# Performance work log

Hardware: AMD Instinct MI355X
Metric: run time of the kernel (lower is better)

## Reference

```python
import jax, jax.numpy as jnp
import numpy as np

N_USER = 100000
N_ITEM = 50000
N = N_USER + N_ITEM
D = 64
E = 4000000
B = 4096
NUM_LAYERS = 2
INT_W = 0.1
POP_W = 0.1
DIS_PEN = 0.01


def setup_inputs() -> dict:
    key = jax.random.key(0)
    ks = jax.random.split(key, 8)
    stdv = 1.0 / np.sqrt(D).astype(np.float32)
    emb_int = jax.random.uniform(ks[0], (N, D), minval=-stdv, maxval=stdv, dtype=jnp.float32)
    emb_pop = jax.random.uniform(ks[1], (N, D), minval=-stdv, maxval=stdv, dtype=jnp.float32)
    user = jax.random.randint(ks[2], (B, 1), 0, N_USER)
    item_p = jax.random.randint(ks[3], (B, 1), 0, N_ITEM)
    item_n = jax.random.randint(ks[4], (B, 1), 0, N_ITEM)
    mask = jax.random.randint(ks[5], (B, 1), 0, 2).astype(bool)
    src = jax.random.randint(ks[6], (E,), 0, N)
    dst = jax.random.randint(ks[7], (E,), 0, N)
    return {"emb_int": emb_int, "emb_pop": emb_pop, "user": user, "item_p": item_p,
            "item_n": item_n, "mask": mask, "src": src, "dst": dst}


def _propagate(emb, src, dst, norm):
    # LightGCN: mean over layer-0..L embeddings, each layer = norm * A @ (norm * h)
    feats = emb
    h = emb
    for _ in range(NUM_LAYERS):
        h = h * norm
        h = jax.ops.segment_sum(h[src], dst, num_segments=N)  # copy_u / sum
        h = h * norm
        feats = feats + h  # dropout p=0 -> identity
    return feats / (NUM_LAYERS + 1)


def reference(emb_int, emb_pop, user, item_p, item_n, mask, src, dst):
    deg = jax.ops.segment_sum(jnp.ones((E,), jnp.float32), dst, num_segments=N)
    norm = jnp.maximum(deg, 1.0) ** -0.5  # [N]
    norm = norm[:, None]  # [N,1]

    f_int = _propagate(emb_int, src, dst, norm)
    f_pop = _propagate(emb_pop, src, dst, norm)

    ip = item_p + N_USER
    inn = item_n + N_USER

    u_int, u_pop = f_int[user], f_pop[user]          # [B,1,D]
    p_int = jnp.sum(u_int * f_int[ip], axis=2)        # [B,1]
    n_int = jnp.sum(u_int * f_int[inn], axis=2)
    p_pop = jnp.sum(u_pop * f_pop[ip], axis=2)
    n_pop = jnp.sum(u_pop * f_pop[inn], axis=2)

    ls = jax.nn.log_sigmoid
    mf = mask.astype(jnp.float32)
    loss_int = -jnp.mean(mf * ls(p_int - n_int))
    loss_pop = -jnp.mean(mf * ls(n_pop - p_pop)) - jnp.mean((1.0 - mf) * ls(p_pop - n_pop))
    loss_total = -jnp.mean(ls((p_int + p_pop) - (n_int + n_pop)))

    # MSE over unique gathered rows == indicator-weighted mean over the table
    item_ind = jnp.zeros((N,), jnp.float32).at[ip.ravel()].set(1.0).at[inn.ravel()].set(1.0)
    user_ind = jnp.zeros((N,), jnp.float32).at[user.ravel()].set(1.0)
    diff2 = (f_int - f_pop) ** 2
    def mse(ind):
        return jnp.sum(ind[:, None] * diff2) / (jnp.sum(ind) * D)
    discrepancy = mse(item_ind) + mse(user_ind)

    return jnp.stack([loss_total, INT_W * loss_int, POP_W * loss_pop, -DIS_PEN * discrepancy])
```

## Files before the change

### kernel.cpp

```cpp
#include <hip/hip_runtime.h>
#include <hip/hip_bf16.h>

typedef unsigned int u32;
typedef float f32x2 __attribute__((ext_vector_type(2)));

#define KNODES 512
#define KSHIFT 9
#define NBMAX 1024
#define CHUNK 4096
#define CAP 16384

__device__ __forceinline__ float log_sigmoid(float x) {
    return fminf(x, 0.f) - log1pf(expf(-fabsf(x)));
}

template <bool HI>
__device__ __forceinline__ f32x2 up8(u32 v) {
    return __builtin_amdgcn_cvt_pk_f32_fp8(v, HI);
}
template <bool HI>
__device__ __forceinline__ u32 pk8(u32 old, float a, float b) {
    return __builtin_amdgcn_cvt_pk_fp8_f32(a, b, old, HI);
}

__global__ void __launch_bounds__(512)
k_scatter(const int* __restrict__ src, const int* __restrict__ dst,
          u32* __restrict__ tails, u32* __restrict__ packed, int E, int nb,
          const int* __restrict__ user, const int* __restrict__ itp,
          const int* __restrict__ itn,
          float* __restrict__ item_ind, float* __restrict__ user_ind,
          int B, int NUSER, const int* __restrict__ maskw, int* __restrict__ flag) {
    __shared__ u32 h[NBMAX];
    const int t = threadIdx.x;
    const int base = blockIdx.x * CHUNK;
    const int PT = CHUNK / 512;
    u32 dv[PT], sv[PT];
#pragma unroll
    for (int i = 0; i < PT; ++i) {
        int e = base + t + i * 512;
        if (e < E) { dv[i] = (u32)dst[e]; sv[i] = (u32)src[e]; }
        else dv[i] = 0xFFFFFFFFu;
    }
    for (int i = t; i < nb; i += 512) h[i] = 0;
    __syncthreads();
#pragma unroll
    for (int i = 0; i < PT; ++i)
        if (dv[i] != 0xFFFFFFFFu) atomicAdd(&h[dv[i] >> KSHIFT], 1u);
    __syncthreads();
    for (int i = t; i < nb; i += 512) {
        u32 c = h[i];
        if (c) h[i] = ((u32)i * CAP) + atomicAdd(&tails[i], c);
    }
    __syncthreads();
#pragma unroll
    for (int i = 0; i < PT; ++i) {
        if (dv[i] != 0xFFFFFFFFu) {
            u32 b = dv[i] >> KSHIFT;
            u32 pos = atomicAdd(&h[b], 1u);
            if (pos < (b + 1u) * CAP)
                packed[pos] = ((dv[i] & (KNODES - 1)) << 18) | sv[i];
        }
    }
    int gid = blockIdx.x * blockDim.x + t;
    int stride = gridDim.x * blockDim.x;
    for (int b = gid; b < B; b += stride) {
        item_ind[itp[b] + NUSER] = 1.f;
        item_ind[itn[b] + NUSER] = 1.f;
        user_ind[user[b]] = 1.f;
    }
    if (blockIdx.x == 0) {
        __shared__ int allok;
        if (t == 0) allok = 1;
        __syncthreads();
        bool ok = true;
        for (int i = t; i < 1024; i += 512) {
            int v = maskw[i];
            if (v != 0 && v != 1) ok = false;
        }
        if (!ok) allok = 0;
        __syncthreads();
        if (t == 0) flag[0] = allok;
    }
}

__global__ void __launch_bounds__(1024)
k_bbuild(const u32* __restrict__ packed, const u32* __restrict__ tails,
         uint2* __restrict__ rowrange, float* __restrict__ norm,
         float* __restrict__ norm2, float* __restrict__ snorm,
         int* __restrict__ csr, int N) {
    __shared__ u32 deg[KNODES], fill[KNODES], sc[KNODES];
    const int t = threadIdx.x;
    const int bkt = blockIdx.x;
    const int nodeBase = bkt << KSHIFT;
    const u32 e0 = (u32)bkt * CAP;
    const u32 e1 = e0 + tails[bkt];
    if (t < KNODES) deg[t] = 0;
    __syncthreads();
    for (u32 e = e0 + t; e < e1; e += 1024)
        atomicAdd(&deg[packed[e] >> 18], 1u);
    __syncthreads();
    u32 dv = (t < KNODES) ? deg[t] : 0u;
    if (t < KNODES) sc[t] = dv;
    __syncthreads();
    for (int off = 1; off < KNODES; off <<= 1) {
        u32 x = 0;
        if (t < KNODES && t >= off) x = sc[t - off];
        __syncthreads();
        if (t < KNODES) sc[t] += x;
        __syncthreads();
    }
    if (t < KNODES) {
        u32 ebase = sc[t] - dv;
        fill[t] = ebase;
        int n = nodeBase + t;
        if (n < N) {
            float dd = fmaxf((float)dv, 1.f);
            float nr = rsqrtf(dd);
            rowrange[n] = make_uint2(e0 + ebase, e0 + ebase + dv);
            norm[n] = nr;
            norm2[n] = nr * nr;
            snorm[n] = sqrtf(dd) * (1.f / 64.f);
        }
    }
    __syncthreads();
    for (u32 e = e0 + t; e < e1; e += 1024) {
        u32 p = packed[e];
        u32 ln = p >> 18;
        u32 pos = atomicAdd(&fill[ln], 1u);
        csr[e0 + pos] = (int)(p & 0x3FFFFu);
    }
}

__global__ void k_pack(const float* __restrict__ eI, const float* __restrict__ eP,
                       const float* __restrict__ norm, u32* __restrict__ T0, int N) {
    int idx = blockIdx.x * blockDim.x + threadIdx.x;
    int total = N * 32;
    int stride = gridDim.x * blockDim.x;
    for (; idx < total; idx += stride) {
        int n = idx >> 5, k = idx & 31;
        const float* e = (k >= 16) ? eP : eI;
        int d0 = (4 * k) & 63;
        float4 v = *(const float4*)&e[(size_t)n * 64 + d0];
        float s = 64.f * norm[n];
        u32 w = 0;
        w = pk8<false>(w, v.x * s, v.y * s);
        w = pk8<true>(w, v.z * s, v.w * s);
        T0[idx] = w;
    }
}

#define ACC8(u) { f32x2 p0 = up8<false>(u.x), p1 = up8<true>(u.x); \
                  f32x2 p2 = up8<false>(u.y), p3 = up8<true>(u.y); \
                  a0 += p0.x; a1 += p0.y; a2 += p1.x; a3 += p1.y;  \
                  a4 += p2.x; a5 += p2.y; a6 += p3.x; a7 += p3.y; }

__global__ void k_pull(const u32* __restrict__ Tin, u32* __restrict__ Tout,
                       const int* __restrict__ csr, const uint2* __restrict__ rowrange,
                       const float* __restrict__ norm2, int N) {
    int lane = threadIdx.x & 63;
    int grp = lane >> 4;
    int r = lane & 15;
    int wid = (blockIdx.x * blockDim.x + threadIdx.x) >> 6;
    int nw = (gridDim.x * blockDim.x) >> 6;
    for (int n = wid; n < N; n += nw) {
        uint2 rr = rowrange[n];
        u32 s0 = rr.x, s1 = rr.y;
        float a0 = 0.f, a1 = 0.f, a2 = 0.f, a3 = 0.f, a4 = 0.f, a5 = 0.f, a6 = 0.f, a7 = 0.f;
        for (u32 e0 = s0; e0 < s1; e0 += 64) {
            int cnt = (int)min(64u, s1 - e0);
            int sidx = (lane < cnt) ? csr[e0 + lane] : 0;
            int j = 0;
            for (; j + 8 <= cnt; j += 8) {
                int sA = __shfl(sidx, j + grp);
                int sB = __shfl(sidx, j + 4 + grp);
                uint2 uA = *(const uint2*)&Tin[(size_t)sA * 32 + 2 * r];
                uint2 uB = *(const uint2*)&Tin[(size_t)sB * 32 + 2 * r];
                ACC8(uA); ACC8(uB);
            }
            for (; j + 4 <= cnt; j += 4) {
                int sA = __shfl(sidx, j + grp);
                uint2 uA = *(const uint2*)&Tin[(size_t)sA * 32 + 2 * r];
                ACC8(uA);
            }
            int rem = cnt - j;
            if (rem) {
                int jj = j + grp;
                int s = __shfl(sidx, (jj < cnt) ? jj : 0);
                if (grp < rem) {
                    uint2 u = *(const uint2*)&Tin[(size_t)s * 32 + 2 * r];
                    ACC8(u);
                }
            }
        }
        a0 += __shfl_xor(a0, 16); a1 += __shfl_xor(a1, 16);
        a2 += __shfl_xor(a2, 16); a3 += __shfl_xor(a3, 16);
        a4 += __shfl_xor(a4, 16); a5 += __shfl_xor(a5, 16);
        a6 += __shfl_xor(a6, 16); a7 += __shfl_xor(a7, 16);
        a0 += __shfl_xor(a0, 32); a1 += __shfl_xor(a1, 32);
        a2 += __shfl_xor(a2, 32); a3 += __shfl_xor(a3, 32);
        a4 += __shfl_xor(a4, 32); a5 += __shfl_xor(a5, 32);
        a6 += __shfl_xor(a6, 32); a7 += __shfl_xor(a7, 32);
        float nn = norm2[n];
        if (lane < 16) {
            u32 w0 = 0, w1 = 0;
            w0 = pk8<false>(w0, a0 * nn, a1 * nn);
            w0 = pk8<true>(w0, a2 * nn, a3 * nn);
            w1 = pk8<false>(w1, a4 * nn, a5 * nn);
            w1 = pk8<true>(w1, a6 * nn, a7 * nn);
            uint2 w; w.x = w0; w.y = w1;
            *(uint2*)&Tout[(size_t)n * 32 + 2 * r] = w;
        }
    }
}

__device__ __forceinline__ void fval2(const float* __restrict__ eb,
                                      const u32* __restrict__ T1, const u32* __restrict__ T2,
                                      const float* __restrict__ snorm,
                                      int r, int toff, int lh, float& f0, float& f1) {
    float2 ev = *(const float2*)&eb[(size_t)r * 64 + 2 * lh];
    u32 w1 = T1[(size_t)r * 32 + toff + (lh >> 1)];
    u32 w2 = T2[(size_t)r * 32 + toff + (lh >> 1)];
    bool hi = lh & 1;
    f32x2 t1 = hi ? up8<true>(w1) : up8<false>(w1);
    f32x2 t2 = hi ? up8<true>(w2) : up8<false>(w2);
    float sr = snorm[r];
    f0 = (ev.x + sr * (t1.x + t2.x)) * (1.f / 3.f);
    f1 = (ev.y + sr * (t1.y + t2.y)) * (1.f / 3.f);
}

__global__ void k_tail(const float* __restrict__ eI, const float* __restrict__ eP,
                       const u32* __restrict__ T1, const u32* __restrict__ T2,
                       const float* __restrict__ snorm,
                       const int* __restrict__ user, const int* __restrict__ itp, const int* __restrict__ itn,
                       const void* __restrict__ maskp, const int* __restrict__ flag,
                       const float* __restrict__ item_ind, const float* __restrict__ user_ind,
                       float* __restrict__ bpart,
                       int B, int NUSER, int N, int Lb, int totalBlocks) {
    __shared__ float part[4][4];
    int lane = threadIdx.x & 63;
    int wib = threadIdx.x >> 6;
    int half = lane >> 5, lh = lane & 31;
    int toff = half ? 16 : 0;
    const float* eb = half ? eP : eI;
    float* row = &bpart[(size_t)blockIdx.x * 8];
    if ((int)blockIdx.x < Lb) {
        int b = (blockIdx.x * blockDim.x + threadIdx.x) >> 6;
        float r0 = 0.f, r1 = 0.f, r2 = 0.f;
        if (b < B) {
            int u = user[b];
            int ip = itp[b] + NUSER;
            int in_ = itn[b] + NUSER;
            float u0, u1, p0, p1, n0, n1;
            fval2(eb, T1, T2, snorm, u,   toff, lh, u0, u1);
            fval2(eb, T1, T2, snorm, ip,  toff, lh, p0, p1);
            fval2(eb, T1, T2, snorm, in_, toff, lh, n0, n1);
            float dp = u0 * p0 + u1 * p1;
            float dn = u0 * n0 + u1 * n1;
            for (int off = 1; off < 32; off <<= 1) {
                dp += __shfl_xor(dp, off);
                dn += __shfl_xor(dn, off);
            }
            float dpI = __shfl(dp, 0), dpP = __shfl(dp, 32);
            float dnI = __shfl(dn, 0), dnP = __shfl(dn, 32);
            if (lane == 0) {
                float m = (*flag) ? (float)(((const int*)maskp)[b] != 0)
                                  : (float)(((const unsigned char*)maskp)[b] != 0);
                r0 = log_sigmoid(dpI + dpP - dnI - dnP);
                r1 = m * log_sigmoid(dpI - dnI);
                r2 = m * log_sigmoid(dnP - dpP) + (1.f - m) * log_sigmoid(dpP - dnP);
            }
        }
        if (lane == 0) { part[wib][0] = r0; part[wib][1] = r1; part[wib][2] = r2; }
        __syncthreads();
        if (threadIdx.x == 0) {
            float s0 = 0.f, s1 = 0.f, s2 = 0.f;
            for (int w = 0; w < 4; ++w) { s0 += part[w][0]; s1 += part[w][1]; s2 += part[w][2]; }
            row[0] = s0; row[1] = s1; row[2] = s2;
            row[3] = 0.f; row[4] = 0.f; row[5] = 0.f; row[6] = 0.f; row[7] = 0.f;
        }
    } else {
        int bid2 = blockIdx.x - Lb;
        int nDb = totalBlocks - Lb;
        int wch = (bid2 * blockDim.x + threadIdx.x) >> 6;
        int nwv = (nDb * blockDim.x) >> 6;
        int nchunks = (N + 63) >> 6;
        float sI = 0.f, sU = 0.f, cI = 0.f, cU = 0.f;
        for (int c = wch; c < nchunks; c += nwv) {
            int base = c << 6;
            int nl = base + lane;
            float ii = (nl < N) ? item_ind[nl] : 0.f;
            float ui = (nl < N) ? user_ind[nl] : 0.f;
            unsigned long long m = __ballot(ii + ui != 0.f);
            while (m) {
                int b = __ffsll((unsigned long long)m) - 1;
                m &= m - 1;
                int n = base + b;
                float iib = __shfl(ii, b);
                float uib = __shfl(ui, b);
                float f0, f1;
                fval2(eb, T1, T2, snorm, n, toff, lh, f0, f1);
                float o0 = __shfl_xor(f0, 32), o1 = __shfl_xor(f1, 32);
                float d0 = f0 - o0, d1 = f1 - o1;
                float dd = d0 * d0 + d1 * d1;
                sI += iib * dd; sU += uib * dd;
                if (lane == 0) { cI += iib; cU += uib; }
            }
        }
        for (int off = 1; off < 64; off <<= 1) { sI += __shfl_xor(sI, off); sU += __shfl_xor(sU, off); }
        if (lane == 0) { part[wib][0] = 0.5f * sI; part[wib][1] = cI; part[wib][2] = 0.5f * sU; part[wib][3] = cU; }
        __syncthreads();
        if (threadIdx.x == 0) {
            float a = 0.f, b = 0.f, c = 0.f, d = 0.f;
            for (int w = 0; w < 4; ++w) { a += part[w][0]; b += part[w][1]; c += part[w][2]; d += part[w][3]; }
            row[0] = 0.f; row[1] = 0.f; row[2] = 0.f;
            row[3] = a; row[4] = b; row[5] = c; row[6] = d; row[7] = 0.f;
        }
    }
}

__global__ void __launch_bounds__(512)
k_final(const float* __restrict__ bpart, float* __restrict__ out, int B, int nblocks) {
    __shared__ float chans[8];
    int lane = threadIdx.x & 63;
    int w = threadIdx.x >> 6;
    if (w < 7) {
        float s = 0.f;
        for (int k = lane; k < nblocks; k += 64)
            s += bpart[(size_t)k * 8 + w];
        for (int off = 1; off < 64; off <<= 1) s += __shfl_xor(s, off);
        if (lane == 0) chans[w] = s;
    }
    __syncthreads();
    if (threadIdx.x == 0) {
        float invB = 1.f / (float)B;
        out[0] = -chans[0] * invB;
        out[1] = -0.1f * chans[1] * invB;
        out[2] = -0.1f * chans[2] * invB;
        float disc = chans[3] / (fmaxf(chans[4], 1.f) * 64.f) + chans[5] / (fmaxf(chans[6], 1.f) * 64.f);
        out[3] = -0.01f * disc;
    }
}

extern "C" void kernel_launch(void* const* d_in, const int* in_sizes, int n_in,
                              void* d_out, int out_size, void* d_ws, size_t ws_size,
                              hipStream_t stream) {
    const float* emb_int = (const float*)d_in[0];
    const float* emb_pop = (const float*)d_in[1];
    const int* user   = (const int*)d_in[2];
    const int* item_p = (const int*)d_in[3];
    const int* item_n = (const int*)d_in[4];
    const void* mask  = d_in[5];
    const int* src    = (const int*)d_in[6];
    const int* dst    = (const int*)d_in[7];

    const int D = 64;
    const int N = in_sizes[0] / D;
    const int B = in_sizes[2];
    const int E = in_sizes[6];
    const int NUSER = 100000;
    const int nb = (N + KNODES - 1) >> KSHIFT;

    char* ws = (char*)d_ws;
    size_t off = 0;
    auto take = [&](size_t bytes) -> void* {
        void* p = ws + off;
        off += (bytes + 255) & ~(size_t)255;
        return p;
    };
    float* acc      = (float*)take(256);
    float* item_ind = (float*)take((size_t)N * 4);
    float* user_ind = (float*)take((size_t)N * 4);
    u32*   tails    = (u32*)take((size_t)nb * 4);
    size_t zero_bytes = off;
    float* bpart    = (float*)take((size_t)4096 * 8 * 4);
    uint2* rowrange = (uint2*)take((size_t)N * 8);
    float* norm     = (float*)take((size_t)N * 4);
    float* norm2    = (float*)take((size_t)N * 4);
    float* snorm    = (float*)take((size_t)N * 4);
    int*   csr      = (int*)take((size_t)nb * CAP * 4);
    u32*   packed   = (u32*)take((size_t)nb * CAP * 4);
    u32*   T0       = (u32*)take((size_t)N * 32 * 4);
    u32*   T1       = (u32*)take((size_t)N * 32 * 4);
    u32*   T2       = (u32*)take((size_t)N * 32 * 4);
    int* flag = (int*)acc + 15;

    (void)hipMemsetAsync(d_ws, 0, zero_bytes, stream);

    k_scatter<<<(E + CHUNK - 1) / CHUNK, 512, 0, stream>>>(src, dst, tails, packed, E, nb,
                                                           user, item_p, item_n,
                                                           item_ind, user_ind, B, NUSER,
                                                           (const int*)mask, flag);
    k_bbuild<<<nb, 1024, 0, stream>>>(packed, tails, rowrange, norm, norm2, snorm, csr, N);
    k_pack<<<2048, 256, 0, stream>>>(emb_int, emb_pop, norm, T0, N);

    k_pull<<<2048, 256, 0, stream>>>(T0, T1, csr, rowrange, norm2, N);
    k_pull<<<2048, 256, 0, stream>>>(T1, T2, csr, rowrange, norm2, N);

    const int Lb = (B * 64 + 255) / 256;
    const int Db = (((N + 63) / 64) + 3) / 4;
    k_tail<<<Lb + Db, 256, 0, stream>>>(emb_int, emb_pop, T1, T2, snorm,
                                        user, item_p, item_n, mask, flag,
                                        item_ind, user_ind, bpart,
                                        B, NUSER, N, Lb, Lb + Db);
    k_final<<<1, 512, 0, stream>>>(bpart, (float*)d_out, B, Lb + Db);
}
```

Baseline: 267.3 us.

## Use 256 non-power-of-two node buckets and widen pull unroll with packed accumulators

Changes CSR bucketing from 512-node power-of-two buckets (about 293 buckets) to exactly 256 buckets of 586 nodes, so the bbuild kernel launches one block per CU with balanced work; the bucket id now comes from an integer division and the packed word is computed during load. The pull kernel unrolls the edge loop to 16 neighbours per iteration and accumulates in f32x2 vectors to allow packed adds. The risks are hard-coded bucket counts that silently assume N <= 256*586 and a per-bucket edge capacity of CAP, plus higher register pressure in the pull loop.

```diff
diff --git a/kernel.cpp b/kernel.cpp
--- a/kernel.cpp
+++ b/kernel.cpp
@@ -4,11 +4,10 @@
 typedef unsigned int u32;
 typedef float f32x2 __attribute__((ext_vector_type(2)));
 
-#define KNODES 512
-#define KSHIFT 9
-#define NBMAX 1024
+#define KN 586
+#define NB 256
 #define CHUNK 4096
-#define CAP 16384
+#define CAP 17408
 
 __device__ __forceinline__ float log_sigmoid(float x) {
     return fminf(x, 0.f) - log1pf(expf(-fabsf(x)));
@@ -25,40 +24,44 @@
 
 __global__ void __launch_bounds__(512)
 k_scatter(const int* __restrict__ src, const int* __restrict__ dst,
-          u32* __restrict__ tails, u32* __restrict__ packed, int E, int nb,
+          u32* __restrict__ tails, u32* __restrict__ packed, int E,
           const int* __restrict__ user, const int* __restrict__ itp,
           const int* __restrict__ itn,
           float* __restrict__ item_ind, float* __restrict__ user_ind,
           int B, int NUSER, const int* __restrict__ maskw, int* __restrict__ flag) {
-    __shared__ u32 h[NBMAX];
+    __shared__ u32 h[NB];
     const int t = threadIdx.x;
     const int base = blockIdx.x * CHUNK;
     const int PT = CHUNK / 512;
-    u32 dv[PT], sv[PT];
+    u32 bv[PT], pv[PT];
 #pragma unroll
     for (int i = 0; i < PT; ++i) {
         int e = base + t + i * 512;
-        if (e < E) { dv[i] = (u32)dst[e]; sv[i] = (u32)src[e]; }
-        else dv[i] = 0xFFFFFFFFu;
-    }
-    for (int i = t; i < nb; i += 512) h[i] = 0;
+        if (e < E) {
+            u32 d = (u32)dst[e];
+            u32 b = d / KN;
+            bv[i] = b;
+            pv[i] = ((d - b * KN) << 18) | (u32)src[e];
+        } else bv[i] = 0xFFFFFFFFu;
+    }
+    if (t < NB) h[t] = 0;
     __syncthreads();
 #pragma unroll
     for (int i = 0; i < PT; ++i)
-        if (dv[i] != 0xFFFFFFFFu) atomicAdd(&h[dv[i] >> KSHIFT], 1u);
-    __syncthreads();
-    for (int i = t; i < nb; i += 512) {
-        u32 c = h[i];
-        if (c) h[i] = ((u32)i * CAP) + atomicAdd(&tails[i], c);
+        if (bv[i] != 0xFFFFFFFFu) atomicAdd(&h[bv[i]], 1u);
+    __syncthreads();
+    if (t < NB) {
+        u32 c = h[t];
+        if (c) h[t] = ((u32)t * CAP) + atomicAdd(&tails[t], c);
     }
     __syncthreads();
 #pragma unroll
     for (int i = 0; i < PT; ++i) {
-        if (dv[i] != 0xFFFFFFFFu) {
-            u32 b = dv[i] >> KSHIFT;
+        if (bv[i] != 0xFFFFFFFFu) {
+            u32 b = bv[i];
             u32 pos = atomicAdd(&h[b], 1u);
             if (pos < (b + 1u) * CAP)
-                packed[pos] = ((dv[i] & (KNODES - 1)) << 18) | sv[i];
+                packed[pos] = pv[i];
         }
     }
     int gid = blockIdx.x * blockDim.x + t;
@@ -88,28 +91,28 @@
          uint2* __restrict__ rowrange, float* __restrict__ norm,
          float* __restrict__ norm2, float* __restrict__ snorm,
          int* __restrict__ csr, int N) {
-    __shared__ u32 deg[KNODES], fill[KNODES], sc[KNODES];
+    __shared__ u32 deg[KN], fill[KN], sc[KN];
     const int t = threadIdx.x;
     const int bkt = blockIdx.x;
-    const int nodeBase = bkt << KSHIFT;
+    const int nodeBase = bkt * KN;
     const u32 e0 = (u32)bkt * CAP;
     const u32 e1 = e0 + tails[bkt];
-    if (t < KNODES) deg[t] = 0;
+    if (t < KN) deg[t] = 0;
     __syncthreads();
     for (u32 e = e0 + t; e < e1; e += 1024)
         atomicAdd(&deg[packed[e] >> 18], 1u);
     __syncthreads();
-    u32 dv = (t < KNODES) ? deg[t] : 0u;
-    if (t < KNODES) sc[t] = dv;
-    __syncthreads();
-    for (int off = 1; off < KNODES; off <<= 1) {
+    u32 dv = (t < KN) ? deg[t] : 0u;
+    if (t < KN) sc[t] = dv;
+    __syncthreads();
+    for (int off = 1; off < 1024; off <<= 1) {
         u32 x = 0;
-        if (t < KNODES && t >= off) x = sc[t - off];
-        __syncthreads();
-        if (t < KNODES) sc[t] += x;
-        __syncthreads();
-    }
-    if (t < KNODES) {
+        if (t < KN && t >= off) x = sc[t - off];
+        __syncthreads();
+        if (t < KN) sc[t] += x;
+        __syncthreads();
+    }
+    if (t < KN) {
         u32 ebase = sc[t] - dv;
         fill[t] = ebase;
         int n = nodeBase + t;
@@ -149,10 +152,8 @@
     }
 }
 
-#define ACC8(u) { f32x2 p0 = up8<false>(u.x), p1 = up8<true>(u.x); \
-                  f32x2 p2 = up8<false>(u.y), p3 = up8<true>(u.y); \
-                  a0 += p0.x; a1 += p0.y; a2 += p1.x; a3 += p1.y;  \
-                  a4 += p2.x; a5 += p2.y; a6 += p3.x; a7 += p3.y; }
+#define ACC8(u) { A0 += up8<false>(u.x); A1 += up8<true>(u.x); \
+                  A2 += up8<false>(u.y); A3 += up8<true>(u.y); }
 
 __global__ void k_pull(const u32* __restrict__ Tin, u32* __restrict__ Tout,
                        const int* __restrict__ csr, const uint2* __restrict__ rowrange,
@@ -165,17 +166,21 @@
     for (int n = wid; n < N; n += nw) {
         uint2 rr = rowrange[n];
         u32 s0 = rr.x, s1 = rr.y;
-        float a0 = 0.f, a1 = 0.f, a2 = 0.f, a3 = 0.f, a4 = 0.f, a5 = 0.f, a6 = 0.f, a7 = 0.f;
+        f32x2 A0 = {0.f, 0.f}, A1 = {0.f, 0.f}, A2 = {0.f, 0.f}, A3 = {0.f, 0.f};
         for (u32 e0 = s0; e0 < s1; e0 += 64) {
             int cnt = (int)min(64u, s1 - e0);
             int sidx = (lane < cnt) ? csr[e0 + lane] : 0;
             int j = 0;
-            for (; j + 8 <= cnt; j += 8) {
+            for (; j + 16 <= cnt; j += 16) {
                 int sA = __shfl(sidx, j + grp);
                 int sB = __shfl(sidx, j + 4 + grp);
+                int sC = __shfl(sidx, j + 8 + grp);
+                int sD = __shfl(sidx, j + 12 + grp);
                 uint2 uA = *(const uint2*)&Tin[(size_t)sA * 32 + 2 * r];
                 uint2 uB = *(const uint2*)&Tin[(size_t)sB * 32 + 2 * r];
-                ACC8(uA); ACC8(uB);
+                uint2 uC = *(const uint2*)&Tin[(size_t)sC * 32 + 2 * r];
+                uint2 uD = *(const uint2*)&Tin[(size_t)sD * 32 + 2 * r];
+                ACC8(uA); ACC8(uB); ACC8(uC); ACC8(uD);
             }
             for (; j + 4 <= cnt; j += 4) {
                 int sA = __shfl(sidx, j + grp);
@@ -192,6 +197,8 @@
                 }
             }
         }
+        float a0 = A0.x, a1 = A0.y, a2 = A1.x, a3 = A1.y;
+        float a4 = A2.x, a5 = A2.y, a6 = A3.x, a7 = A3.y;
         a0 += __shfl_xor(a0, 16); a1 += __shfl_xor(a1, 16);
         a2 += __shfl_xor(a2, 16); a3 += __shfl_xor(a3, 16);
         a4 += __shfl_xor(a4, 16); a5 += __shfl_xor(a5, 16);
@@ -358,7 +365,6 @@
     const int B = in_sizes[2];
     const int E = in_sizes[6];
     const int NUSER = 100000;
-    const int nb = (N + KNODES - 1) >> KSHIFT;
 
     char* ws = (char*)d_ws;
     size_t off = 0;
@@ -370,15 +376,15 @@
     float* acc      = (float*)take(256);
     float* item_ind = (float*)take((size_t)N * 4);
     float* user_ind = (float*)take((size_t)N * 4);
-    u32*   tails    = (u32*)take((size_t)nb * 4);
+    u32*   tails    = (u32*)take((size_t)NB * 4);
     size_t zero_bytes = off;
     float* bpart    = (float*)take((size_t)4096 * 8 * 4);
     uint2* rowrange = (uint2*)take((size_t)N * 8);
     float* norm     = (float*)take((size_t)N * 4);
     float* norm2    = (float*)take((size_t)N * 4);
     float* snorm    = (float*)take((size_t)N * 4);
-    int*   csr      = (int*)take((size_t)nb * CAP * 4);
-    u32*   packed   = (u32*)take((size_t)nb * CAP * 4);
+    int*   csr      = (int*)take((size_t)NB * CAP * 4);
+    u32*   packed   = (u32*)take((size_t)NB * CAP * 4);
     u32*   T0       = (u32*)take((size_t)N * 32 * 4);
     u32*   T1       = (u32*)take((size_t)N * 32 * 4);
     u32*   T2       = (u32*)take((size_t)N * 32 * 4);
@@ -386,11 +392,11 @@
 
     (void)hipMemsetAsync(d_ws, 0, zero_bytes, stream);
 
-    k_scatter<<<(E + CHUNK - 1) / CHUNK, 512, 0, stream>>>(src, dst, tails, packed, E, nb,
+    k_scatter<<<(E + CHUNK - 1) / CHUNK, 512, 0, stream>>>(src, dst, tails, packed, E,
                                                            user, item_p, item_n,
                                                            item_ind, user_ind, B, NUSER,
                                                            (const int*)mask, flag);
-    k_bbuild<<<nb, 1024, 0, stream>>>(packed, tails, rowrange, norm, norm2, snorm, csr, N);
+    k_bbuild<<<NB, 1024, 0, stream>>>(packed, tails, rowrange, norm, norm2, snorm, csr, N);
     k_pack<<<2048, 256, 0, stream>>>(emb_int, emb_pop, norm, T0, N);
 
     k_pull<<<2048, 256, 0, stream>>>(T0, T1, csr, rowrange, norm2, N);
```

After: 261.7 us. 1.02x faster.
